# Kernel optimization log

Measured on AMD Instinct MI355X. Metric: run time of the kernel, lower is better.

Reference implementation:

```python
import jax, jax.numpy as jnp
import numpy as np
from jax import lax

B, C, T, H, W = 4, 64, 80, 36, 64
N = 128   # ntargets
NT = 10   # temporal taps


def setup_inputs() -> dict:
    key = jax.random.key(0)
    ks = jax.random.split(key, 8)
    x = jax.random.normal(ks[0], (B, C, T, H, W), dtype=jnp.float32)
    targets = jnp.ones((1, N), dtype=bool)
    wc = ((0.1 * jax.random.normal(ks[1], (C, N)) / 10 + 1) / C).astype(jnp.float32)
    wx = (-0.4 + 0.8 * jax.random.uniform(ks[2], (N,))).astype(jnp.float32)
    wy = (-0.4 + 0.8 * jax.random.uniform(ks[3], (N,))).astype(jnp.float32)
    wsigmax = (0.5 + 0.1 * jax.random.uniform(ks[4], (N,))).astype(jnp.float32)
    wsigmay = (0.5 + 0.1 * jax.random.uniform(ks[5], (N,))).astype(jnp.float32)
    wt = ((1 + 0.1 * jax.random.normal(ks[6], (NT, N))) / NT).astype(jnp.float32)
    wb = (jax.random.normal(ks[7], (N,)) * 0.05 + 0.6).astype(jnp.float32)
    return {"x": x, "targets": targets, "wc": wc, "wx": wx, "wy": wy,
            "wsigmax": wsigmax, "wsigmay": wsigmay, "wt": wt, "wb": wb}


def reference(x, targets, wc, wx, wy, wsigmax, wsigmay, wt, wb):
    b, c, t, h, w = x.shape
    n = wc.shape[1]
    # spatial grids in [-0.5, 0.5), matching torch.meshgrid(indexing='ij')
    yv = (jnp.arange(h, dtype=jnp.float32) - h / 2 + 0.5) / h
    xv = (jnp.arange(w, dtype=jnp.float32) - w / 2 + 0.5) / w
    ygrid, xgrid = jnp.meshgrid(yv, xv, indexing='ij')  # [h, w]

    # Gaussian soft-pooling weights ws: [h*w, n]
    sx = 0.1 + jax.nn.relu(wsigmax) ** 2
    sy = 0.1 + jax.nn.relu(wsigmay) ** 2
    dx = (xgrid.reshape(-1, 1) - wx[None, :]) ** 2 / (2.0 * sx[None, :])
    dy = (ygrid.reshape(-1, 1) - wy[None, :]) ** 2 / (2.0 * sy[None, :])
    ws = jnp.exp(-dx - dy)
    ws = ws / (0.1 + ws.sum(axis=0, keepdims=True))

    # subnet = identity; flatten (batch, time) -> frames, channels x space
    x2 = x.transpose(0, 2, 1, 3, 4).reshape(b * t, c, h * w)  # [bt, c, s]
    # fused channel mix (wc) + spatial soft-pool (ws): out[f, n]
    R = jnp.einsum('fcs,cn,sn->fn', x2, wc, ws, optimize=True)  # [b*t, n]
    R = R.reshape(b, t, n).transpose(0, 2, 1)  # [b, n, t]

    # grouped temporal conv1d (cross-correlation, VALID), one kernel per target
    kern = wt.T[:, None, :]  # [n, 1, nt]
    out = lax.conv_general_dilated(
        R, kern, window_strides=(1,), padding='VALID',
        dimension_numbers=('NCH', 'OIH', 'NCH'), feature_group_count=n)
    return out + wb[None, :, None]  # [b, n, t - nt + 1]
```

## Files before the change

kernel.cpp:

```cpp
#include <hip/hip_runtime.h>
#include <hip/hip_bf16.h>
#include <stdint.h>

#define B_ 4
#define C_ 64
#define T_ 80
#define H_ 36
#define W_ 64
#define N_ 128
#define NT_ 10
#define S_ (H_*W_)
#define M_ (B_*C_*T_)
#define K_ S_
#define TOUT (T_-NT_+1)

#define BM 32
#define BK 64
#define KSPLIT 2
#define NIT (K_ / (BK * KSPLIT))

using float4v = __attribute__((ext_vector_type(4))) float;
using short8v = __attribute__((ext_vector_type(8))) short;

__device__ __forceinline__ unsigned short f2bf(float f) {
  unsigned int u = __float_as_uint(f);
  u += 0x7fffu + ((u >> 16) & 1u);
  return (unsigned short)(u >> 16);
}

__device__ __forceinline__ unsigned int pkbf(float a, float b) {
  union { __hip_bfloat162 h2; unsigned int u; } cv;
  cv.h2 = __float22bfloat162_rn(make_float2(a, b));
  return cv.u;
}

__device__ __forceinline__ void glds16(const void* g, void* l) {
  __builtin_amdgcn_global_load_lds(
      (const __attribute__((address_space(1))) unsigned int*)g,
      (__attribute__((address_space(3))) unsigned int*)l, 16, 0, 0);
}

__global__ __launch_bounds__(256) void k1_ws(const float* __restrict__ wx,
                                             const float* __restrict__ wy,
                                             const float* __restrict__ wsigx,
                                             const float* __restrict__ wsigy,
                                             unsigned short* __restrict__ Bp) {
  const int n = blockIdx.x;
  const int tid = threadIdx.x;
  const float cx = wx[n], cy = wy[n];
  const float rx = fmaxf(wsigx[n], 0.f);
  const float ry = fmaxf(wsigy[n], 0.f);
  const float i2sx = 0.5f / (0.1f + rx * rx);
  const float i2sy = 0.5f / (0.1f + ry * ry);

  float ev[9];
  float part = 0.f;
#pragma unroll
  for (int i = 0; i < 9; ++i) {
    const int s = tid + i * 256;
    const int h = s >> 6, w = s & 63;
    const float dx = (w - 31.5f) * (1.f / 64.f) - cx;
    const float dy = (h - 17.5f) * (1.f / 36.f) - cy;
    const float e = __expf(-(dx * dx * i2sx + dy * dy * i2sy));
    ev[i] = e;
    part += e;
  }
#pragma unroll
  for (int off = 32; off > 0; off >>= 1) part += __shfl_down(part, off);
  __shared__ float red[4];
  if ((tid & 63) == 0) red[tid >> 6] = part;
  __syncthreads();
  const float inv = 1.f / (0.1f + red[0] + red[1] + red[2] + red[3]);
#pragma unroll
  for (int i = 0; i < 9; ++i) {
    const int s = tid + i * 256;
    Bp[((s >> 3) * N_ + n) * 8 + (s & 7)] = f2bf(ev[i] * inv);
  }
}

__global__ __launch_bounds__(256, 4) void k2_gemm(const float* __restrict__ A,
                                                  const unsigned short* __restrict__ Bp,
                                                  float* __restrict__ Zp) {
  __shared__ float4v As[2][BM * 16];
  const int tid = threadIdx.x;
  const int lane = tid & 63;
  const int wv = tid >> 6;
  const int m15 = lane & 15;
  const int q = lane >> 4;
  const int mBase = blockIdx.x * BM;
  const int split = blockIdx.y;
  const int kStart = split * (K_ / KSPLIT);

  const float* ga[2];
  int lam_[2];
#pragma unroll
  for (int i = 0; i < 2; ++i) {
    const int lam = i * 256 + tid;
    const int r = lam >> 4;
    const int c4 = (lam & 15) ^ (r & 15);
    ga[i] = A + (size_t)(mBase + r) * K_ + kStart + c4 * 4;
    lam_[i] = lam;
  }

  float4v acc[2][2];
#pragma unroll
  for (int i = 0; i < 2; ++i)
#pragma unroll
    for (int j = 0; j < 2; ++j) acc[i][j] = (float4v)(0.f);

#pragma unroll
  for (int i = 0; i < 2; ++i) glds16(ga[i], &As[0][lam_[i]]);

  int cur = 0;
  for (int it = 0; it < NIT; ++it) {
    __syncthreads();
    if (it + 1 < NIT) {
#pragma unroll
      for (int i = 0; i < 2; ++i)
        glds16(ga[i] + (size_t)(it + 1) * BK, &As[cur ^ 1][lam_[i]]);
    }
    const int kg0 = (kStart + it * BK) >> 3;
#pragma unroll
    for (int ks = 0; ks < 2; ++ks) {
      const int c4a = ks * 8 + q * 2;
      union { short8v s8; unsigned int u[4]; } af[2];
#pragma unroll
      for (int mt = 0; mt < 2; ++mt) {
        const int rowc = (mt * 16 + m15) * 16;
        const float4v alo = As[cur][rowc + (c4a ^ m15)];
        const float4v ahi = As[cur][rowc + ((c4a + 1) ^ m15)];
        af[mt].u[0] = pkbf(alo[0], alo[1]);
        af[mt].u[1] = pkbf(alo[2], alo[3]);
        af[mt].u[2] = pkbf(ahi[0], ahi[1]);
        af[mt].u[3] = pkbf(ahi[2], ahi[3]);
      }
      const int kg = kg0 + ks * 4 + q;
#pragma unroll
      for (int nt = 0; nt < 2; ++nt) {
        const int col = wv * 32 + nt * 16 + m15;
        const short8v bf =
            *(const short8v*)(Bp + ((size_t)kg * N_ + col) * 8);
        acc[0][nt] = __builtin_amdgcn_mfma_f32_16x16x32_bf16(af[0].s8, bf, acc[0][nt], 0, 0, 0);
        acc[1][nt] = __builtin_amdgcn_mfma_f32_16x16x32_bf16(af[1].s8, bf, acc[1][nt], 0, 0, 0);
      }
    }
    cur ^= 1;
  }

  float* Z = Zp + (size_t)split * M_ * N_;
#pragma unroll
  for (int mt = 0; mt < 2; ++mt)
#pragma unroll
    for (int nt = 0; nt < 2; ++nt)
#pragma unroll
      for (int v = 0; v < 4; ++v)
        Z[(size_t)(mBase + mt * 16 + q * 4 + v) * N_ + wv * 32 + nt * 16 + m15] =
            acc[mt][nt][v];
}

__global__ __launch_bounds__(128) void k3_reduce_c(const float* __restrict__ Zp,
                                                   const float* __restrict__ wc,
                                                   float* __restrict__ R) {
  const int n = threadIdx.x;
  const int bt = blockIdx.x;
  const int b = bt / T_;
  const int t = bt - b * T_;
  const float* Z0 = Zp;
  const float* Z1 = Zp + (size_t)M_ * N_;
  float s = 0.f;
#pragma unroll 8
  for (int c = 0; c < C_; ++c) {
    const size_t idx = (size_t)((b * C_ + c) * T_ + t) * N_ + n;
    s += (Z0[idx] + Z1[idx]) * wc[c * N_ + n];
  }
  R[(b * T_ + t) * N_ + n] = s;
}

__global__ __launch_bounds__(128) void k4_conv(const float* __restrict__ R,
                                               const float* __restrict__ wt,
                                               const float* __restrict__ wb,
                                               float* __restrict__ out) {
  const int n = threadIdx.x;
  const int tau = blockIdx.x;
  const int b = blockIdx.y;
  float s = wb[n];
#pragma unroll
  for (int j = 0; j < NT_; ++j) {
    s += R[(b * T_ + tau + j) * N_ + n] * wt[j * N_ + n];
  }
  out[((size_t)b * N_ + n) * TOUT + tau] = s;
}

extern "C" void kernel_launch(void* const* d_in, const int* in_sizes, int n_in,
                              void* d_out, int out_size, void* d_ws, size_t ws_size,
                              hipStream_t stream) {
  (void)in_sizes; (void)n_in; (void)out_size; (void)ws_size;
  const float* x    = (const float*)d_in[0];
  const float* wc   = (const float*)d_in[2];
  const float* wx   = (const float*)d_in[3];
  const float* wy   = (const float*)d_in[4];
  const float* wsx  = (const float*)d_in[5];
  const float* wsy  = (const float*)d_in[6];
  const float* wt   = (const float*)d_in[7];
  const float* wb   = (const float*)d_in[8];
  float* out = (float*)d_out;

  char* ws = (char*)d_ws;
  unsigned short* Bp = (unsigned short*)ws;
  float* R = (float*)(ws + 589824);
  float* Zp = (float*)(ws + 589824 + 163840);

  k1_ws<<<N_, 256, 0, stream>>>(wx, wy, wsx, wsy, Bp);
  dim3 g2(M_ / BM, KSPLIT);
  k2_gemm<<<g2, 256, 0, stream>>>(x, Bp, Zp);
  k3_reduce_c<<<B_ * T_, 128, 0, stream>>>(Zp, wc, R);
  dim3 g4(TOUT, B_);
  k4_conv<<<g4, 128, 0, stream>>>(R, wt, wb, out);
}
```

Before: 297.0 us.

## Fuse channel reduction with wc into GEMM epilogue using per-frame tiles and atomics

Each GEMM block now covers one (batch,time) frame and all 64 channels (BM=64). The epilogue multiplies its accumulators by wc, reduces across lanes, and atomically adds into R. This removes the large Zp intermediate write and re-read as well as the separate reduce kernel, and the K-split grows to 4 to keep enough blocks. The cost is a memset of R, float atomics, and strided per-frame row gathers from x.

```diff
diff --git a/kernel.cpp b/kernel.cpp
--- a/kernel.cpp
+++ b/kernel.cpp
@@ -14,10 +14,11 @@
 #define K_ S_
 #define TOUT (T_-NT_+1)
 
-#define BM 32
+#define BM 64
 #define BK 64
-#define KSPLIT 2
-#define NIT (K_ / (BK * KSPLIT))
+#define KSPLIT 4
+#define KCH (K_ / KSPLIT)
+#define NIT (KCH / BK)
 
 using float4v = __attribute__((ext_vector_type(4))) float;
 using short8v = __attribute__((ext_vector_type(8))) short;
@@ -78,102 +79,89 @@
   }
 }
 
-__global__ __launch_bounds__(256, 4) void k2_gemm(const float* __restrict__ A,
-                                                  const unsigned short* __restrict__ Bp,
-                                                  float* __restrict__ Zp) {
+__global__ __launch_bounds__(256, 4) void k2_fused(const float* __restrict__ A,
+                                                   const unsigned short* __restrict__ Bp,
+                                                   const float* __restrict__ wc,
+                                                   float* __restrict__ R) {
   __shared__ float4v As[2][BM * 16];
   const int tid = threadIdx.x;
   const int lane = tid & 63;
   const int wv = tid >> 6;
   const int m15 = lane & 15;
   const int q = lane >> 4;
-  const int mBase = blockIdx.x * BM;
+  const int bt = blockIdx.x;
+  const int b = bt / T_;
+  const int t = bt - b * T_;
   const int split = blockIdx.y;
-  const int kStart = split * (K_ / KSPLIT);
-
-  const float* ga[2];
-  int lam_[2];
-#pragma unroll
-  for (int i = 0; i < 2; ++i) {
+  const int kStart = split * KCH;
+
+  const float* ga[4];
+  int lam_[4];
+#pragma unroll
+  for (int i = 0; i < 4; ++i) {
     const int lam = i * 256 + tid;
     const int r = lam >> 4;
     const int c4 = (lam & 15) ^ (r & 15);
-    ga[i] = A + (size_t)(mBase + r) * K_ + kStart + c4 * 4;
+    ga[i] = A + (size_t)((b * C_ + r) * T_ + t) * K_ + kStart + c4 * 4;
     lam_[i] = lam;
   }
 
-  float4v acc[2][2];
-#pragma unroll
-  for (int i = 0; i < 2; ++i)
+  float4v acc[4][2];
+#pragma unroll
+  for (int i = 0; i < 4; ++i)
 #pragma unroll
     for (int j = 0; j < 2; ++j) acc[i][j] = (float4v)(0.f);
 
 #pragma unroll
-  for (int i = 0; i < 2; ++i) glds16(ga[i], &As[0][lam_[i]]);
+  for (int i = 0; i < 4; ++i) glds16(ga[i], &As[0][lam_[i]]);
 
   int cur = 0;
   for (int it = 0; it < NIT; ++it) {
     __syncthreads();
     if (it + 1 < NIT) {
 #pragma unroll
-      for (int i = 0; i < 2; ++i)
+      for (int i = 0; i < 4; ++i)
         glds16(ga[i] + (size_t)(it + 1) * BK, &As[cur ^ 1][lam_[i]]);
     }
     const int kg0 = (kStart + it * BK) >> 3;
 #pragma unroll
     for (int ks = 0; ks < 2; ++ks) {
+      const int kg = kg0 + ks * 4 + q;
+      const short8v bf0 =
+          *(const short8v*)(Bp + ((size_t)kg * N_ + wv * 32 + m15) * 8);
+      const short8v bf1 =
+          *(const short8v*)(Bp + ((size_t)kg * N_ + wv * 32 + 16 + m15) * 8);
       const int c4a = ks * 8 + q * 2;
-      union { short8v s8; unsigned int u[4]; } af[2];
-#pragma unroll
-      for (int mt = 0; mt < 2; ++mt) {
+#pragma unroll
+      for (int mt = 0; mt < 4; ++mt) {
         const int rowc = (mt * 16 + m15) * 16;
         const float4v alo = As[cur][rowc + (c4a ^ m15)];
         const float4v ahi = As[cur][rowc + ((c4a + 1) ^ m15)];
-        af[mt].u[0] = pkbf(alo[0], alo[1]);
-        af[mt].u[1] = pkbf(alo[2], alo[3]);
-        af[mt].u[2] = pkbf(ahi[0], ahi[1]);
-        af[mt].u[3] = pkbf(ahi[2], ahi[3]);
-      }
-      const int kg = kg0 + ks * 4 + q;
-#pragma unroll
-      for (int nt = 0; nt < 2; ++nt) {
-        const int col = wv * 32 + nt * 16 + m15;
-        const short8v bf =
-            *(const short8v*)(Bp + ((size_t)kg * N_ + col) * 8);
-        acc[0][nt] = __builtin_amdgcn_mfma_f32_16x16x32_bf16(af[0].s8, bf, acc[0][nt], 0, 0, 0);
-        acc[1][nt] = __builtin_amdgcn_mfma_f32_16x16x32_bf16(af[1].s8, bf, acc[1][nt], 0, 0, 0);
+        union { short8v s8; unsigned int u[4]; } af;
+        af.u[0] = pkbf(alo[0], alo[1]);
+        af.u[1] = pkbf(alo[2], alo[3]);
+        af.u[2] = pkbf(ahi[0], ahi[1]);
+        af.u[3] = pkbf(ahi[2], ahi[3]);
+        acc[mt][0] = __builtin_amdgcn_mfma_f32_16x16x32_bf16(af.s8, bf0, acc[mt][0], 0, 0, 0);
+        acc[mt][1] = __builtin_amdgcn_mfma_f32_16x16x32_bf16(af.s8, bf1, acc[mt][1], 0, 0, 0);
       }
     }
     cur ^= 1;
   }
 
-  float* Z = Zp + (size_t)split * M_ * N_;
-#pragma unroll
-  for (int mt = 0; mt < 2; ++mt)
-#pragma unroll
-    for (int nt = 0; nt < 2; ++nt)
+#pragma unroll
+  for (int nt = 0; nt < 2; ++nt) {
+    const int n = wv * 32 + nt * 16 + m15;
+    float p = 0.f;
+#pragma unroll
+    for (int mt = 0; mt < 4; ++mt)
 #pragma unroll
       for (int v = 0; v < 4; ++v)
-        Z[(size_t)(mBase + mt * 16 + q * 4 + v) * N_ + wv * 32 + nt * 16 + m15] =
-            acc[mt][nt][v];
-}
-
-__global__ __launch_bounds__(128) void k3_reduce_c(const float* __restrict__ Zp,
-                                                   const float* __restrict__ wc,
-                                                   float* __restrict__ R) {
-  const int n = threadIdx.x;
-  const int bt = blockIdx.x;
-  const int b = bt / T_;
-  const int t = bt - b * T_;
-  const float* Z0 = Zp;
-  const float* Z1 = Zp + (size_t)M_ * N_;
-  float s = 0.f;
-#pragma unroll 8
-  for (int c = 0; c < C_; ++c) {
-    const size_t idx = (size_t)((b * C_ + c) * T_ + t) * N_ + n;
-    s += (Z0[idx] + Z1[idx]) * wc[c * N_ + n];
-  }
-  R[(b * T_ + t) * N_ + n] = s;
+        p += acc[mt][nt][v] * wc[(mt * 16 + q * 4 + v) * N_ + n];
+    p += __shfl_xor(p, 16);
+    p += __shfl_xor(p, 32);
+    if (q == 0) atomicAdd(&R[(size_t)bt * N_ + n], p);
+  }
 }
 
 __global__ __launch_bounds__(128) void k4_conv(const float* __restrict__ R,
@@ -208,12 +196,11 @@
   char* ws = (char*)d_ws;
   unsigned short* Bp = (unsigned short*)ws;
   float* R = (float*)(ws + 589824);
-  float* Zp = (float*)(ws + 589824 + 163840);
-
+
+  hipMemsetAsync(R, 0, (size_t)B_ * T_ * N_ * sizeof(float), stream);
   k1_ws<<<N_, 256, 0, stream>>>(wx, wy, wsx, wsy, Bp);
-  dim3 g2(M_ / BM, KSPLIT);
-  k2_gemm<<<g2, 256, 0, stream>>>(x, Bp, Zp);
-  k3_reduce_c<<<B_ * T_, 128, 0, stream>>>(Zp, wc, R);
+  dim3 g2(B_ * T_, KSPLIT);
+  k2_fused<<<g2, 256, 0, stream>>>(x, Bp, wc, R);
   dim3 g4(TOUT, B_);
   k4_conv<<<g4, 128, 0, stream>>>(R, wt, wb, out);
 }
```

New measurement: 285.7 us. 3.8% less time.
